# Kernel tuning notes

Measured on AMD Instinct MI355X. Metric: run time of the kernel, lower is better.

## Reference

```python
import jax, jax.numpy as jnp
import numpy as np

B, D, E, H, DEPTH, NH, K = 4, 384, 8, 1536, 12, 6, 2
P, NTOK = 16, 197  # patch size, 14*14 patches + cls
EPS = 1e-6


def layernorm(x, w, b):
    m = x.mean(-1, keepdims=True)
    v = ((x - m) ** 2).mean(-1, keepdims=True)
    return (x - m) / jnp.sqrt(v + EPS) * w + b


def attention(x, qkv_w, qkv_b, proj_w, proj_b):
    Bn, N, C = x.shape
    hd = C // NH
    qkv = x @ qkv_w.T + qkv_b                       # [B,N,3C]
    qkv = qkv.reshape(Bn, N, 3, NH, hd).transpose(2, 0, 3, 1, 4)
    q, k, v = qkv[0], qkv[1], qkv[2]                # [B,h,N,hd]
    attn = jax.nn.softmax((q @ k.transpose(0, 1, 3, 2)) * (hd ** -0.5), axis=-1)
    out = (attn @ v).transpose(0, 2, 1, 3).reshape(Bn, N, C)
    return out @ proj_w.T + proj_b


def mlp(x, w1, b1, w2, b2):
    h = jax.nn.gelu(x @ w1.T + b1, approximate=False)
    return h @ w2.T + b2


def moe_ffn(x2d, gw, w1, b1, w2, b2):
    # noiseless top-k gating (eval mode of NoisyTopKGating)
    logits = x2d @ gw                                # [T,E]
    T = logits.shape[0]
    top_vals, top_idx = jax.lax.top_k(logits, K + 1)
    gates_k = jax.nn.softmax(top_vals[:, :K], axis=-1)
    gates = jnp.zeros((T, E), x2d.dtype).at[jnp.arange(T)[:, None], top_idx[:, :K]].set(gates_k)
    # dense per-expert FFN, weighted combine (identical math to SparseDispatcher)
    h = jax.nn.gelu(jnp.einsum('td,edh->teh', x2d, w1) + b1, approximate=False)
    out = jnp.einsum('teh,ehd->ted', h, w2) + b2
    return jnp.einsum('te,ted->td', gates, out)


def forward(x, patch_w, patch_b, cls_token, pos_embed,
            ln1_w, ln1_b, qkv_w, qkv_b, proj_w, proj_b, ln2_w, ln2_b,
            fc1_w, fc1_b, fc2_w, fc2_b,
            gate_w, moe_w1, moe_b1, moe_w2, moe_b2, lnf_w, lnf_b):
    # patch embed: conv k=16 s=16
    feat = jax.lax.conv_general_dilated(x, patch_w, (P, P), 'VALID',
                                        dimension_numbers=('NCHW', 'OIHW', 'NCHW'))
    feat = feat + patch_b[None, :, None, None]
    Bn = feat.shape[0]
    tokens = feat.reshape(Bn, D, -1).transpose(0, 2, 1)          # [B,196,D]
    cls = jnp.broadcast_to(cls_token, (Bn, 1, D))
    h = jnp.concatenate([cls, tokens], axis=1) + pos_embed       # [B,197,D]

    for i in range(DEPTH):
        h = h + attention(layernorm(h, ln1_w[i], ln1_b[i]), qkv_w[i], qkv_b[i], proj_w[i], proj_b[i])
        y = layernorm(h, ln2_w[i], ln2_b[i])
        if i % 2 == 1:
            j = i // 2
            y2 = moe_ffn(y.reshape(-1, D), gate_w[j], moe_w1[j], moe_b1[j], moe_w2[j], moe_b2[j])
            h = h + y2.reshape(Bn, NTOK, D)
        else:
            j = i // 2
            h = h + mlp(y, fc1_w[j], fc1_b[j], fc2_w[j], fc2_b[j])
    return layernorm(h, lnf_w, lnf_b)


def setup_inputs() -> dict:
    key = jax.random.key(0)
    ks = jax.random.split(key, 16)
    rn = lambda k, s, sd=0.02: jax.random.normal(k, s, jnp.float32) * sd
    return {
        'x': jax.random.normal(ks[0], (B, 3, 224, 224), jnp.float32),
        'patch_w': rn(ks[1], (D, 3, P, P)), 'patch_b': jnp.zeros((D,), jnp.float32),
        'cls_token': rn(ks[2], (1, 1, D)), 'pos_embed': rn(ks[3], (1, NTOK, D)),
        'ln1_w': jnp.ones((DEPTH, D), jnp.float32), 'ln1_b': jnp.zeros((DEPTH, D), jnp.float32),
        'qkv_w': rn(ks[4], (DEPTH, 3 * D, D)), 'qkv_b': jnp.zeros((DEPTH, 3 * D), jnp.float32),
        'proj_w': rn(ks[5], (DEPTH, D, D)), 'proj_b': jnp.zeros((DEPTH, D), jnp.float32),
        'ln2_w': jnp.ones((DEPTH, D), jnp.float32), 'ln2_b': jnp.zeros((DEPTH, D), jnp.float32),
        'fc1_w': rn(ks[6], (DEPTH // 2, H, D)), 'fc1_b': jnp.zeros((DEPTH // 2, H), jnp.float32),
        'fc2_w': rn(ks[7], (DEPTH // 2, D, H)), 'fc2_b': jnp.zeros((DEPTH // 2, D), jnp.float32),
        'gate_w': rn(ks[8], (DEPTH // 2, D, E)),
        'moe_w1': rn(ks[9], (DEPTH // 2, E, D, H)), 'moe_b1': jnp.zeros((DEPTH // 2, E, H), jnp.float32),
        'moe_w2': rn(ks[10], (DEPTH // 2, E, H, D)), 'moe_b2': jnp.zeros((DEPTH // 2, E, D), jnp.float32),
        'lnf_w': jnp.ones((D,), jnp.float32), 'lnf_b': jnp.zeros((D,), jnp.float32),
    }


def reference(x, patch_w, patch_b, cls_token, pos_embed,
              ln1_w, ln1_b, qkv_w, qkv_b, proj_w, proj_b, ln2_w, ln2_b,
              fc1_w, fc1_b, fc2_w, fc2_b,
              gate_w, moe_w1, moe_b1, moe_w2, moe_b2, lnf_w, lnf_b):
    return forward(x, patch_w, patch_b, cls_token, pos_embed,
                   ln1_w, ln1_b, qkv_w, qkv_b, proj_w, proj_b, ln2_w, ln2_b,
                   fc1_w, fc1_b, fc2_w, fc2_b,
                   gate_w, moe_w1, moe_b1, moe_w2, moe_b2, lnf_w, lnf_b)
```

## Files before the change

kernel.cpp:

```cpp
#include <hip/hip_runtime.h>
#include <math.h>

#define NBATCH 4
#define NTOK 197
#define TT 788
#define DM 384
#define HM 1536
#define NHEAD 6
#define NEXP 8
#define LD2 72
#define MOUTSZ (TT * 2 * DM)

typedef __attribute__((ext_vector_type(8))) short bf16x8;
typedef __attribute__((ext_vector_type(4))) float f32x4;

__device__ __forceinline__ void f2bf2(float x, short& hi, short& lo) {
    unsigned u = __float_as_uint(x);
    unsigned uh = u + (0x7fffu + ((u >> 16) & 1u));
    hi = (short)(uh >> 16);
    float hf = __uint_as_float(uh & 0xffff0000u);
    float r = x - hf;
    unsigned v = __float_as_uint(r);
    lo = (short)((v + (0x7fffu + ((v >> 16) & 1u))) >> 16);
}
__device__ __forceinline__ float gelu_f(float x) {
    return 0.5f * x * (1.0f + erff(x * 0.7071067811865475f));
}

__global__ void k_im2col(const float* __restrict__ X, float* __restrict__ P) {
    int p = blockIdx.x;
    int b = p / 196, pp = p % 196;
    int py = pp / 14, px = pp % 14;
    const float* xb = X + (size_t)b * 3 * 224 * 224;
    float* dst = P + (size_t)p * 768;
    for (int idx = threadIdx.x; idx < 768; idx += 256) {
        int c = idx >> 8;
        int i = (idx >> 4) & 15;
        int j = idx & 15;
        dst[idx] = xb[((size_t)c * 224 + py * 16 + i) * 224 + px * 16 + j];
    }
}

__global__ void k_assemble(const float* __restrict__ PO, const float* __restrict__ pb,
                           const float* __restrict__ cls, const float* __restrict__ pos,
                           float* __restrict__ H) {
    int t = blockIdx.x;
    int b = t / NTOK, n = t % NTOK;
    for (int d = threadIdx.x; d < DM; d += 128) {
        float v;
        if (n == 0) v = cls[d];
        else v = PO[((size_t)b * 196 + (n - 1)) * DM + d] + pb[d];
        H[(size_t)t * DM + d] = v + pos[(size_t)n * DM + d];
    }
}

__global__ void k_ln(const float* __restrict__ X, const float* __restrict__ w,
                     const float* __restrict__ b, float* __restrict__ Y) {
    int t = blockIdx.x, lane = threadIdx.x;
    const float* x = X + (size_t)t * DM;
    float v[6];
    float s = 0.f;
    #pragma unroll
    for (int i = 0; i < 6; ++i) { v[i] = x[lane + i * 64]; s += v[i]; }
    #pragma unroll
    for (int off = 32; off; off >>= 1) s += __shfl_xor(s, off);
    float mean = s * (1.f / 384.f);
    float q = 0.f;
    #pragma unroll
    for (int i = 0; i < 6; ++i) { float d = v[i] - mean; q += d * d; }
    #pragma unroll
    for (int off = 32; off; off >>= 1) q += __shfl_xor(q, off);
    float inv = rsqrtf(q * (1.f / 384.f) + 1e-6f);
    float* y = Y + (size_t)t * DM;
    #pragma unroll
    for (int i = 0; i < 6; ++i) {
        int d = lane + i * 64;
        y[d] = (v[i] - mean) * inv * w[d] + b[d];
    }
}

__global__ __launch_bounds__(256) void k_gemm_mfma(
    const float* __restrict__ A, const float* __restrict__ W,
    const float* __restrict__ bias, float* __restrict__ C,
    int M, int N, int K, int flags, int MT, int NT, int wprot, int ksplit,
    const float* __restrict__ lnw, const float* __restrict__ lnb)
{
    int mt, nt, ks = 0;
    {
        int lane8 = blockIdx.x & 7;
        int idx = blockIdx.x >> 3;
        if (ksplit > 1) { ks = idx % ksplit; idx /= ksplit; }
        if (wprot) {
            mt = idx % MT;
            nt = lane8 + 8 * (idx / MT);
            if (nt >= NT) return;
        } else {
            nt = idx % NT;
            mt = lane8 + 8 * (idx / NT);
            if (mt >= MT) return;
        }
    }
    const int Ks = K / ksplit;
    const float* Ab = A + (size_t)ks * Ks;
    const float* Wb = W + (size_t)ks * Ks;
    __shared__ short Ah[64 * LD2], Al[64 * LD2], Bh[64 * LD2], Bl[64 * LD2];
    const int bm = mt * 64, bn = nt * 64;
    const int tid = threadIdx.x;
    const int lane = tid & 63, w = tid >> 6;
    const int wr = w >> 1, wc = w & 1;
    const int r16 = lane & 15, g = lane >> 4;
    const int sr = tid >> 4;
    const int sc = (tid & 15) * 4;
    const bool doln = (flags & 8) != 0;
    float am[4], ai[4];
    #pragma unroll
    for (int p = 0; p < 4; ++p) { am[p] = 0.f; ai[p] = 1.f; }
    if (doln) {
        int j = tid & 15;
        #pragma unroll
        for (int p = 0; p < 4; ++p) {
            int r = bm + sr + p * 16;
            if (r < M) {
                const float* xr = A + (size_t)r * K;
                float s = 0.f, ss = 0.f;
                #pragma unroll
                for (int i = 0; i < 6; ++i) {
                    float4 v = *(const float4*)(xr + j * 4 + i * 64);
                    s += v.x + v.y + v.z + v.w;
                    ss += v.x * v.x + v.y * v.y + v.z * v.z + v.w * v.w;
                }
                #pragma unroll
                for (int off = 1; off < 16; off <<= 1) {
                    s += __shfl_xor(s, off);
                    ss += __shfl_xor(ss, off);
                }
                float mean = s * (1.f / 384.f);
                float var = ss * (1.f / 384.f) - mean * mean;
                am[p] = mean;
                ai[p] = rsqrtf(var + 1e-6f);
            }
        }
    }
    float4 ra[4], rb[4], lw4, lb4;
    auto LOADT = [&](int k0) {
        if (doln) {
            lw4 = *(const float4*)(lnw + k0 + sc);
            lb4 = *(const float4*)(lnb + k0 + sc);
        }
        #pragma unroll
        for (int p = 0; p < 4; ++p) {
            int r = sr + p * 16;
            ra[p] = make_float4(0.f, 0.f, 0.f, 0.f);
            if (bm + r < M) ra[p] = *(const float4*)(Ab + (size_t)(bm + r) * K + k0 + sc);
            rb[p] = *(const float4*)(Wb + (size_t)(bn + r) * K + k0 + sc);
        }
    };
    auto STORET = [&]() {
        #pragma unroll
        for (int p = 0; p < 4; ++p) {
            int r = sr + p * 16;
            float4 a4 = ra[p];
            if (doln) {
                a4.x = (a4.x - am[p]) * ai[p] * lw4.x + lb4.x;
                a4.y = (a4.y - am[p]) * ai[p] * lw4.y + lb4.y;
                a4.z = (a4.z - am[p]) * ai[p] * lw4.z + lb4.z;
                a4.w = (a4.w - am[p]) * ai[p] * lw4.w + lb4.w;
            }
            float4 b4 = rb[p];
            short4 ah, al, bh, bl;
            f2bf2(a4.x, ah.x, al.x); f2bf2(a4.y, ah.y, al.y);
            f2bf2(a4.z, ah.z, al.z); f2bf2(a4.w, ah.w, al.w);
            f2bf2(b4.x, bh.x, bl.x); f2bf2(b4.y, bh.y, bl.y);
            f2bf2(b4.z, bh.z, bl.z); f2bf2(b4.w, bh.w, bl.w);
            *(short4*)&Ah[r * LD2 + sc] = ah; *(short4*)&Al[r * LD2 + sc] = al;
            *(short4*)&Bh[r * LD2 + sc] = bh; *(short4*)&Bl[r * LD2 + sc] = bl;
        }
    };
    f32x4 acc[2][2] = {};
    auto COMPUTE = [&]() {
        #pragma unroll
        for (int kk = 0; kk < 2; ++kk) {
            bf16x8 afh[2], afl[2], bfh[2], bfl[2];
            #pragma unroll
            for (int i = 0; i < 2; ++i) {
                int off = (wr * 32 + i * 16 + r16) * LD2 + kk * 32 + g * 8;
                afh[i] = *(const bf16x8*)&Ah[off];
                afl[i] = *(const bf16x8*)&Al[off];
            }
            #pragma unroll
            for (int j = 0; j < 2; ++j) {
                int off = (wc * 32 + j * 16 + r16) * LD2 + kk * 32 + g * 8;
                bfh[j] = *(const bf16x8*)&Bh[off];
                bfl[j] = *(const bf16x8*)&Bl[off];
            }
            #pragma unroll
            for (int i = 0; i < 2; ++i)
                #pragma unroll
                for (int j = 0; j < 2; ++j) {
                    acc[i][j] = __builtin_amdgcn_mfma_f32_16x16x32_bf16(afl[i], bfh[j], acc[i][j], 0, 0, 0);
                    acc[i][j] = __builtin_amdgcn_mfma_f32_16x16x32_bf16(afh[i], bfl[j], acc[i][j], 0, 0, 0);
                    acc[i][j] = __builtin_amdgcn_mfma_f32_16x16x32_bf16(afh[i], bfh[j], acc[i][j], 0, 0, 0);
                }
        }
    };
    LOADT(0);
    STORET();
    __syncthreads();
    for (int k0 = 64; k0 < Ks; k0 += 64) {
        LOADT(k0);
        COMPUTE();
        __syncthreads();
        STORET();
        __syncthreads();
    }
    COMPUTE();
    #pragma unroll
    for (int i = 0; i < 2; ++i) {
        #pragma unroll
        for (int j = 0; j < 2; ++j) {
            int n = bn + wc * 32 + j * 16 + r16;
            float bb = (bias && ks == 0) ? bias[n] : 0.f;
            int mbase = bm + wr * 32 + i * 16 + g * 4;
            #pragma unroll
            for (int r = 0; r < 4; ++r) {
                int m = mbase + r;
                if (m < M) {
                    float v = acc[i][j][r] + bb;
                    float* cp = C + (size_t)m * N + n;
                    if (flags & 16) {
                        atomicAdd(cp, v);
                    } else {
                        if (flags & 1) v = gelu_f(v);
                        if (flags & 2) v += *cp;
                        *cp = v;
                    }
                }
            }
        }
    }
}

__global__ __launch_bounds__(256) void k_scoresm(const float* __restrict__ QKV,
                                                 float* __restrict__ S) {
    int z = blockIdx.y;
    int b = z / NHEAD, hh = z % NHEAD;
    int i0 = blockIdx.x * 32;
    __shared__ float qs[32][65];
    __shared__ float ks[32][65];
    __shared__ float srow[32][200];
    int tid = threadIdx.x;
    int r = tid >> 3, d0 = (tid & 7) * 8, c0 = (tid & 7) * 4, l8 = tid & 7;
    {
        float4 v0 = make_float4(0,0,0,0), v1 = v0;
        if (i0 + r < NTOK) {
            const float* qp = QKV + ((size_t)(b * NTOK + i0 + r)) * 1152 + hh * 64 + d0;
            v0 = *(const float4*)qp; v1 = *(const float4*)(qp + 4);
        }
        qs[r][d0+0]=v0.x; qs[r][d0+1]=v0.y; qs[r][d0+2]=v0.z; qs[r][d0+3]=v0.w;
        qs[r][d0+4]=v1.x; qs[r][d0+5]=v1.y; qs[r][d0+6]=v1.z; qs[r][d0+7]=v1.w;
    }
    if (l8 == 0) { srow[r][197] = -1e30f; srow[r][198] = -1e30f; srow[r][199] = -1e30f; }
    for (int j0 = 0; j0 < NTOK; j0 += 32) {
        __syncthreads();
        {
            float4 v0 = make_float4(0,0,0,0), v1 = v0;
            if (j0 + r < NTOK) {
                const float* kp = QKV + ((size_t)(b * NTOK + j0 + r)) * 1152 + 384 + hh * 64 + d0;
                v0 = *(const float4*)kp; v1 = *(const float4*)(kp + 4);
            }
            ks[r][d0+0]=v0.x; ks[r][d0+1]=v0.y; ks[r][d0+2]=v0.z; ks[r][d0+3]=v0.w;
            ks[r][d0+4]=v1.x; ks[r][d0+5]=v1.y; ks[r][d0+6]=v1.z; ks[r][d0+7]=v1.w;
        }
        __syncthreads();
        float acc[4] = {0.f, 0.f, 0.f, 0.f};
        #pragma unroll 8
        for (int d = 0; d < 64; ++d) {
            float qv = qs[r][d];
            #pragma unroll
            for (int u = 0; u < 4; ++u) acc[u] += qv * ks[c0 + u][d];
        }
        #pragma unroll
        for (int u = 0; u < 4; ++u) {
            int j = j0 + c0 + u;
            if (j < NTOK) srow[r][j] = acc[u] * 0.125f;
        }
    }
    __syncthreads();
    float m = -1e30f;
    for (int c = l8; c < 200; c += 8) m = fmaxf(m, srow[r][c]);
    #pragma unroll
    for (int off = 1; off < 8; off <<= 1) m = fmaxf(m, __shfl_xor(m, off));
    float s = 0.f;
    for (int c = l8; c < 200; c += 8) {
        float e = expf(srow[r][c] - m);
        srow[r][c] = e;
        s += e;
    }
    #pragma unroll
    for (int off = 1; off < 8; off <<= 1) s += __shfl_xor(s, off);
    float invs = 1.f / s;
    int i = i0 + r;
    if (i < NTOK) {
        float* sp = S + ((size_t)z * NTOK + i) * NTOK;
        for (int c = l8; c < NTOK; c += 8) sp[c] = srow[r][c] * invs;
    }
}

__global__ __launch_bounds__(256) void k_pv(const float* __restrict__ S, const float* __restrict__ QKV,
                                            float* __restrict__ AO) {
    int z = blockIdx.y;
    int b = z / NHEAD, hh = z % NHEAD;
    int i0 = blockIdx.x * 32;
    __shared__ float ps[32][33];
    __shared__ float vs[32][65];
    int tid = threadIdx.x;
    int r = tid >> 3;
    int c4 = (tid & 7) * 4;
    int d0 = (tid & 7) * 8;
    float acc[8] = {};
    for (int k0 = 0; k0 < NTOK; k0 += 32) {
        #pragma unroll
        for (int u = 0; u < 4; ++u) {
            int i = i0 + r, j = k0 + c4 + u;
            ps[r][c4 + u] = (i < NTOK && j < NTOK) ? S[((size_t)z * NTOK + i) * NTOK + j] : 0.f;
        }
        {
            float4 v0 = make_float4(0,0,0,0), v1 = v0;
            if (k0 + r < NTOK) {
                const float* vp = QKV + ((size_t)(b * NTOK + k0 + r)) * 1152 + 768 + hh * 64 + d0;
                v0 = *(const float4*)vp; v1 = *(const float4*)(vp + 4);
            }
            vs[r][d0+0]=v0.x; vs[r][d0+1]=v0.y; vs[r][d0+2]=v0.z; vs[r][d0+3]=v0.w;
            vs[r][d0+4]=v1.x; vs[r][d0+5]=v1.y; vs[r][d0+6]=v1.z; vs[r][d0+7]=v1.w;
        }
        __syncthreads();
        #pragma unroll 8
        for (int kk = 0; kk < 32; ++kk) {
            float pw = ps[r][kk];
            #pragma unroll
            for (int j = 0; j < 8; ++j) acc[j] += pw * vs[kk][d0 + j];
        }
        __syncthreads();
    }
    int i = i0 + r;
    if (i < NTOK) {
        float* op = AO + (size_t)(b * NTOK + i) * DM + hh * 64 + d0;
        #pragma unroll
        for (int j = 0; j < 8; ++j) op[j] = acc[j];
    }
}

__global__ void k_route_ln(const float* __restrict__ H, float* __restrict__ lnstat,
                           const float* __restrict__ lnw, const float* __restrict__ lnb,
                           const float* __restrict__ GW,
                           int* __restrict__ eidx, float* __restrict__ egate) {
    int t = blockIdx.x * 4 + (threadIdx.x >> 6);
    if (t >= TT) return;
    int lane = threadIdx.x & 63;
    const float* x = H + (size_t)t * DM;
    float v[6];
    float s = 0.f, ss = 0.f;
    #pragma unroll
    for (int i = 0; i < 6; ++i) {
        v[i] = x[lane + i * 64];
        s += v[i];
        ss += v[i] * v[i];
    }
    #pragma unroll
    for (int off = 32; off; off >>= 1) { s += __shfl_xor(s, off); ss += __shfl_xor(ss, off); }
    float mean = s * (1.f / 384.f);
    float var = ss * (1.f / 384.f) - mean * mean;
    float inv = rsqrtf(var + 1e-6f);
    if (lane == 0) { lnstat[2 * t] = mean; lnstat[2 * t + 1] = inv; }
    float l8v[NEXP] = {};
    #pragma unroll
    for (int i = 0; i < 6; ++i) {
        int d = lane + i * 64;
        float yv = (v[i] - mean) * inv * lnw[d] + lnb[d];
        const float* g = GW + (size_t)d * NEXP;
        #pragma unroll
        for (int e = 0; e < NEXP; ++e) l8v[e] += yv * g[e];
    }
    #pragma unroll
    for (int e = 0; e < NEXP; ++e) {
        float vv = l8v[e];
        #pragma unroll
        for (int off = 32; off; off >>= 1) vv += __shfl_xor(vv, off);
        l8v[e] = vv;
    }
    if (lane == 0) {
        int b0 = 0;
        #pragma unroll
        for (int e = 1; e < NEXP; ++e) if (l8v[e] > l8v[b0]) b0 = e;
        int b1 = -1;
        #pragma unroll
        for (int e = 0; e < NEXP; ++e) if (e != b0 && (b1 < 0 || l8v[e] > l8v[b1])) b1 = e;
        float e1 = expf(l8v[b1] - l8v[b0]);
        float denom = 1.f + e1;
        eidx[2 * t] = b0; eidx[2 * t + 1] = b1;
        egate[2 * t] = 1.f / denom; egate[2 * t + 1] = e1 / denom;
    }
}

__global__ void k_pscatter(int* __restrict__ cnt, int* __restrict__ basep,
                           const int* __restrict__ eidx,
                           int* __restrict__ slot_tok, int* __restrict__ slot_of) {
    __shared__ int hist[NEXP];
    __shared__ int bp[NEXP];
    __shared__ int fl[NEXP];
    int tid = threadIdx.x;
    if (tid < NEXP) { hist[tid] = 0; fl[tid] = 0; }
    __syncthreads();
    for (int i = tid; i < 2 * TT; i += 256) atomicAdd(&hist[eidx[i]], 1);
    __syncthreads();
    if (tid == 0) {
        int s = 0;
        for (int e = 0; e < NEXP; ++e) { bp[e] = s; s += hist[e]; }
    }
    __syncthreads();
    if (tid < NEXP) { cnt[tid] = hist[tid]; basep[tid] = bp[tid]; }
    for (int t = tid; t < TT; t += 256) {
        #pragma unroll
        for (int k = 0; k < 2; ++k) {
            int e = eidx[2 * t + k];
            int pos = atomicAdd(&fl[e], 1);
            int s = bp[e] + pos;
            slot_tok[s] = t;
            slot_of[2 * t + k] = s;
        }
    }
}

__global__ __launch_bounds__(256) void k_moe1_mfma(
    const float* __restrict__ H, const float* __restrict__ lnstat,
    const float* __restrict__ lnw, const float* __restrict__ lnb,
    const float* __restrict__ W1, const float* __restrict__ B1,
    const int* __restrict__ slot_tok, const int* __restrict__ cnt, const int* __restrict__ basep,
    float* __restrict__ HID)
{
    const int e = blockIdx.x & 7;
    const int idx = blockIdx.x >> 3;
    const int mt = idx % 13;
    const int nt = idx / 13;
    const int c = cnt[e];
    const int r0 = mt * 64;
    if (r0 >= c) return;
    const int sbase = basep[e];
    const int n0 = nt * 64;
    const float* W = W1 + (size_t)e * DM * HM;
    const float* B1e = B1 + (size_t)e * HM;
    __shared__ short Ah[64 * LD2], Al[64 * LD2], Bh[64 * LD2], Bl[64 * LD2];
    const int tid = threadIdx.x;
    const int lane = tid & 63, w = tid >> 6;
    const int wr = w >> 1, wc = w & 1;
    const int r16 = lane & 15, g = lane >> 4;
    const int sr = tid >> 4, sc = (tid & 15) * 4;
    const int kq = (tid >> 4) * 4;
    int tokp[4];
    float am4[4], ai4[4];
    #pragma unroll
    for (int p = 0; p < 4; ++p) {
        int m = r0 + sr + p * 16;
        tokp[p] = (m < c) ? slot_tok[sbase + m] : -1;
        am4[p] = 0.f; ai4[p] = 1.f;
        if (tokp[p] >= 0) { am4[p] = lnstat[2 * tokp[p]]; ai4[p] = lnstat[2 * tokp[p] + 1]; }
    }
    f32x4 acc[2][2] = {};
    for (int k0 = 0; k0 < DM; k0 += 64) {
        float4 lw4 = *(const float4*)(lnw + k0 + sc);
        float4 lb4 = *(const float4*)(lnb + k0 + sc);
        #pragma unroll
        for (int p = 0; p < 4; ++p) {
            int r = sr + p * 16;
            float4 a4 = make_float4(0.f, 0.f, 0.f, 0.f);
            if (tokp[p] >= 0) {
                a4 = *(const float4*)(H + (size_t)tokp[p] * DM + k0 + sc);
                a4.x = (a4.x - am4[p]) * ai4[p] * lw4.x + lb4.x;
                a4.y = (a4.y - am4[p]) * ai4[p] * lw4.y + lb4.y;
                a4.z = (a4.z - am4[p]) * ai4[p] * lw4.z + lb4.z;
                a4.w = (a4.w - am4[p]) * ai4[p] * lw4.w + lb4.w;
            }
            short4 ah, al;
            f2bf2(a4.x, ah.x, al.x); f2bf2(a4.y, ah.y, al.y);
            f2bf2(a4.z, ah.z, al.z); f2bf2(a4.w, ah.w, al.w);
            *(short4*)&Ah[r * LD2 + sc] = ah; *(short4*)&Al[r * LD2 + sc] = al;
        }
        {
            float4 b4[4];
            #pragma unroll
            for (int i = 0; i < 4; ++i)
                b4[i] = *(const float4*)(W + (size_t)(k0 + kq + i) * HM + n0 + sc);
            float col[4][4] = {
                { b4[0].x, b4[1].x, b4[2].x, b4[3].x },
                { b4[0].y, b4[1].y, b4[2].y, b4[3].y },
                { b4[0].z, b4[1].z, b4[2].z, b4[3].z },
                { b4[0].w, b4[1].w, b4[2].w, b4[3].w } };
            #pragma unroll
            for (int u = 0; u < 4; ++u) {
                short4 hh, ll;
                f2bf2(col[u][0], hh.x, ll.x); f2bf2(col[u][1], hh.y, ll.y);
                f2bf2(col[u][2], hh.z, ll.z); f2bf2(col[u][3], hh.w, ll.w);
                *(short4*)&Bh[(sc + u) * LD2 + kq] = hh;
                *(short4*)&Bl[(sc + u) * LD2 + kq] = ll;
            }
        }
        __syncthreads();
        #pragma unroll
        for (int kk = 0; kk < 2; ++kk) {
            bf16x8 afh[2], afl[2], bfh[2], bfl[2];
            #pragma unroll
            for (int i = 0; i < 2; ++i) {
                int off = (wr * 32 + i * 16 + r16) * LD2 + kk * 32 + g * 8;
                afh[i] = *(const bf16x8*)&Ah[off];
                afl[i] = *(const bf16x8*)&Al[off];
            }
            #pragma unroll
            for (int j = 0; j < 2; ++j) {
                int off = (wc * 32 + j * 16 + r16) * LD2 + kk * 32 + g * 8;
                bfh[j] = *(const bf16x8*)&Bh[off];
                bfl[j] = *(const bf16x8*)&Bl[off];
            }
            #pragma unroll
            for (int i = 0; i < 2; ++i)
                #pragma unroll
                for (int j = 0; j < 2; ++j) {
                    acc[i][j] = __builtin_amdgcn_mfma_f32_16x16x32_bf16(afl[i], bfh[j], acc[i][j], 0, 0, 0);
                    acc[i][j] = __builtin_amdgcn_mfma_f32_16x16x32_bf16(afh[i], bfl[j], acc[i][j], 0, 0, 0);
                    acc[i][j] = __builtin_amdgcn_mfma_f32_16x16x32_bf16(afh[i], bfh[j], acc[i][j], 0, 0, 0);
                }
        }
        __syncthreads();
    }
    #pragma unroll
    for (int i = 0; i < 2; ++i) {
        #pragma unroll
        for (int j = 0; j < 2; ++j) {
            int n = n0 + wc * 32 + j * 16 + r16;
            float bb = B1e[n];
            #pragma unroll
            for (int r = 0; r < 4; ++r) {
                int m = r0 + wr * 32 + i * 16 + g * 4 + r;
                if (m < c)
                    HID[(size_t)(sbase + m) * HM + n] = gelu_f(acc[i][j][r] + bb);
            }
        }
    }
}

__global__ __launch_bounds__(256) void k_moe2_mfma(
    const float* __restrict__ HID, const float* __restrict__ W2,
    const int* __restrict__ cnt, const int* __restrict__ basep,
    float* __restrict__ MOUTP)
{
    const int e = blockIdx.x & 7;
    const int idx = blockIdx.x >> 3;
    const int mt = idx % 13;
    const int rest = idx / 13;
    const int nt = rest % 6;
    const int ks = rest / 6;
    const int c = cnt[e];
    const int r0 = mt * 64;
    if (r0 >= c) return;
    const int sbase = basep[e];
    const int n0 = nt * 64;
    const int kbase = ks * 384;
    const float* W = W2 + (size_t)e * HM * DM + (size_t)kbase * DM;
    float* outp = MOUTP + (size_t)ks * MOUTSZ;
    __shared__ short Ah[64 * LD2], Al[64 * LD2], Bh[64 * LD2], Bl[64 * LD2];
    const int tid = threadIdx.x;
    const int lane = tid & 63, w = tid >> 6;
    const int wr = w >> 1, wc = w & 1;
    const int r16 = lane & 15, g = lane >> 4;
    const int sr = tid >> 4, sc = (tid & 15) * 4;
    const int kq = (tid >> 4) * 4;
    f32x4 acc[2][2] = {};
    for (int k0 = 0; k0 < 384; k0 += 64) {
        #pragma unroll
        for (int p = 0; p < 4; ++p) {
            int r = sr + p * 16;
            int m = r0 + r;
            float4 a4 = make_float4(0.f, 0.f, 0.f, 0.f);
            if (m < c) a4 = *(const float4*)(HID + (size_t)(sbase + m) * HM + kbase + k0 + sc);
            short4 ah, al;
            f2bf2(a4.x, ah.x, al.x); f2bf2(a4.y, ah.y, al.y);
            f2bf2(a4.z, ah.z, al.z); f2bf2(a4.w, ah.w, al.w);
            *(short4*)&Ah[r * LD2 + sc] = ah; *(short4*)&Al[r * LD2 + sc] = al;
        }
        {
            float4 b4[4];
            #pragma unroll
            for (int i = 0; i < 4; ++i)
                b4[i] = *(const float4*)(W + (size_t)(k0 + kq + i) * DM + n0 + sc);
            float col[4][4] = {
                { b4[0].x, b4[1].x, b4[2].x, b4[3].x },
                { b4[0].y, b4[1].y, b4[2].y, b4[3].y },
                { b4[0].z, b4[1].z, b4[2].z, b4[3].z },
                { b4[0].w, b4[1].w, b4[2].w, b4[3].w } };
            #pragma unroll
            for (int u = 0; u < 4; ++u) {
                short4 hh, ll;
                f2bf2(col[u][0], hh.x, ll.x); f2bf2(col[u][1], hh.y, ll.y);
                f2bf2(col[u][2], hh.z, ll.z); f2bf2(col[u][3], hh.w, ll.w);
                *(short4*)&Bh[(sc + u) * LD2 + kq] = hh;
                *(short4*)&Bl[(sc + u) * LD2 + kq] = ll;
            }
        }
        __syncthreads();
        #pragma unroll
        for (int kk = 0; kk < 2; ++kk) {
            bf16x8 afh[2], afl[2], bfh[2], bfl[2];
            #pragma unroll
            for (int i = 0; i < 2; ++i) {
                int off = (wr * 32 + i * 16 + r16) * LD2 + kk * 32 + g * 8;
                afh[i] = *(const bf16x8*)&Ah[off];
                afl[i] = *(const bf16x8*)&Al[off];
            }
            #pragma unroll
            for (int j = 0; j < 2; ++j) {
                int off = (wc * 32 + j * 16 + r16) * LD2 + kk * 32 + g * 8;
                bfh[j] = *(const bf16x8*)&Bh[off];
                bfl[j] = *(const bf16x8*)&Bl[off];
            }
            #pragma unroll
            for (int i = 0; i < 2; ++i)
                #pragma unroll
                for (int j = 0; j < 2; ++j) {
                    acc[i][j] = __builtin_amdgcn_mfma_f32_16x16x32_bf16(afl[i], bfh[j], acc[i][j], 0, 0, 0);
                    acc[i][j] = __builtin_amdgcn_mfma_f32_16x16x32_bf16(afh[i], bfl[j], acc[i][j], 0, 0, 0);
                    acc[i][j] = __builtin_amdgcn_mfma_f32_16x16x32_bf16(afh[i], bfh[j], acc[i][j], 0, 0, 0);
                }
        }
        __syncthreads();
    }
    #pragma unroll
    for (int i = 0; i < 2; ++i) {
        #pragma unroll
        for (int j = 0; j < 2; ++j) {
            int n = n0 + wc * 32 + j * 16 + r16;
            #pragma unroll
            for (int r = 0; r < 4; ++r) {
                int m = r0 + wr * 32 + i * 16 + g * 4 + r;
                if (m < c)
                    outp[(size_t)(sbase + m) * DM + n] = acc[i][j][r];
            }
        }
    }
}

__global__ void k_combine(const float* __restrict__ MOUTP, const int* __restrict__ slot_of,
                          const int* __restrict__ eidx, const float* __restrict__ egate,
                          const float* __restrict__ B2, float* __restrict__ H) {
    int t = blockIdx.x;
    int s0 = slot_of[2 * t], s1 = slot_of[2 * t + 1];
    int e0 = eidx[2 * t], e1 = eidx[2 * t + 1];
    float g0 = egate[2 * t], g1 = egate[2 * t + 1];
    for (int d = threadIdx.x; d < DM; d += 128) {
        float v0 = B2[(size_t)e0 * DM + d];
        float v1 = B2[(size_t)e1 * DM + d];
        #pragma unroll
        for (int p = 0; p < 4; ++p) {
            v0 += MOUTP[(size_t)p * MOUTSZ + (size_t)s0 * DM + d];
            v1 += MOUTP[(size_t)p * MOUTSZ + (size_t)s1 * DM + d];
        }
        H[(size_t)t * DM + d] += g0 * v0 + g1 * v1;
    }
}

extern "C" void kernel_launch(void* const* d_in, const int* in_sizes, int n_in,
                              void* d_out, int out_size, void* d_ws, size_t ws_size,
                              hipStream_t stream) {
    const float* x         = (const float*)d_in[0];
    const float* patch_w   = (const float*)d_in[1];
    const float* patch_b   = (const float*)d_in[2];
    const float* cls_token = (const float*)d_in[3];
    const float* pos_embed = (const float*)d_in[4];
    const float* ln1_w     = (const float*)d_in[5];
    const float* ln1_b     = (const float*)d_in[6];
    const float* qkv_w     = (const float*)d_in[7];
    const float* qkv_b     = (const float*)d_in[8];
    const float* proj_w    = (const float*)d_in[9];
    const float* proj_b    = (const float*)d_in[10];
    const float* ln2_w     = (const float*)d_in[11];
    const float* ln2_b     = (const float*)d_in[12];
    const float* fc1_w     = (const float*)d_in[13];
    const float* fc1_b     = (const float*)d_in[14];
    const float* fc2_w     = (const float*)d_in[15];
    const float* fc2_b     = (const float*)d_in[16];
    const float* gate_w    = (const float*)d_in[17];
    const float* moe_w1    = (const float*)d_in[18];
    const float* moe_b1    = (const float*)d_in[19];
    const float* moe_w2    = (const float*)d_in[20];
    const float* moe_b2    = (const float*)d_in[21];
    const float* lnf_w     = (const float*)d_in[22];
    const float* lnf_b     = (const float*)d_in[23];
    float* out = (float*)d_out;

    float* wsf = (float*)d_ws;
    float* regA     = wsf;
    float* patches  = regA;
    float* patchout = regA + 602112;
    float* moehid   = regA;
    float* h     = regA + 2420736;
    float* spare = h + 302592;
    float* qkvb  = spare + 302592;
    float* attno = qkvb + 907776;
    float* regC  = attno + 302592;
    float* S    = regC;
    float* hid  = regC;
    float* mout4 = qkvb;
    float* egate = regC + 1210368;
    int* ib       = (int*)(egate + 1576);
    int* eidx     = ib;
    int* slot_tok = ib + 1576;
    int* slot_of  = ib + 3152;
    int* cnt      = ib + 4728;
    int* basep    = ib + 4736;
    float* lnstat = (float*)(ib + 4752);

    k_im2col<<<784, 256, 0, stream>>>(x, patches);
    k_gemm_mfma<<<96, 256, 0, stream>>>(patches, patch_w, nullptr, patchout,
                                        784, DM, 768, 0, 13, 6, 0, 1, nullptr, nullptr);
    k_assemble<<<TT, 128, 0, stream>>>(patchout, patch_b, cls_token, pos_embed, h);

    for (int l = 0; l < 12; ++l) {
        k_gemm_mfma<<<312, 256, 0, stream>>>(h, qkv_w + (size_t)l * 1152 * DM,
                                             qkv_b + l * 1152, qkvb, TT, 1152, DM, 8,
                                             13, 18, 1, 1,
                                             ln1_w + l * DM, ln1_b + l * DM);
        k_scoresm<<<dim3(7, NBATCH * NHEAD), 256, 0, stream>>>(qkvb, S);
        k_pv<<<dim3(7, NBATCH * NHEAD), 256, 0, stream>>>(S, qkvb, attno);
        k_gemm_mfma<<<192, 256, 0, stream>>>(attno, proj_w + (size_t)l * DM * DM,
                                             proj_b + l * DM, h, TT, DM, DM, 16,
                                             13, 6, 0, 2, nullptr, nullptr);
        int j = l >> 1;
        if ((l & 1) == 0) {
            k_gemm_mfma<<<312, 256, 0, stream>>>(h, fc1_w + (size_t)j * HM * DM,
                                                 fc1_b + j * HM, hid, TT, HM, DM, 9,
                                                 13, 24, 1, 1,
                                                 ln2_w + l * DM, ln2_b + l * DM);
            k_gemm_mfma<<<384, 256, 0, stream>>>(hid, fc2_w + (size_t)j * DM * HM,
                                                 fc2_b + j * DM, h, TT, DM, HM, 16,
                                                 13, 6, 0, 4, nullptr, nullptr);
        } else {
            k_route_ln<<<197, 256, 0, stream>>>(h, lnstat, ln2_w + l * DM, ln2_b + l * DM,
                                                gate_w + (size_t)j * DM * NEXP, eidx, egate);
            k_pscatter<<<1, 256, 0, stream>>>(cnt, basep, eidx, slot_tok, slot_of);
            k_moe1_mfma<<<8 * 13 * 24, 256, 0, stream>>>(
                h, lnstat, ln2_w + l * DM, ln2_b + l * DM,
                moe_w1 + (size_t)j * NEXP * DM * HM, moe_b1 + (size_t)j * NEXP * HM,
                slot_tok, cnt, basep, moehid);
            k_moe2_mfma<<<8 * 13 * 24, 256, 0, stream>>>(
                moehid, moe_w2 + (size_t)j * NEXP * HM * DM, cnt, basep, mout4);
            k_combine<<<TT, 128, 0, stream>>>(mout4, slot_of, eidx, egate,
                                              moe_b2 + (size_t)j * NEXP * DM, h);
        }
    }
    k_ln<<<TT, 64, 0, stream>>>(h, lnf_w, lnf_b, out);
}
```

Measured before the change: 1.669 ms.

## Fuse im2col and assembly into patch GEMM; fold MoE combine into expert GEMM atomics

A dedicated patch-embedding GEMM now reads image patches straight from the input and writes tokens with patch bias, position embedding and the cls row. This replaces the im2col, generic GEMM and assembly kernels. The MoE second-expert GEMM now scales its outputs by per-slot gates and atomically adds them into the residual stream, which removes the split-K partial buffer and the combine kernel. The cost is fp32 atomics onto shared rows, which also makes the summation order non-deterministic.

```diff
diff --git a/kernel.cpp b/kernel.cpp
--- a/kernel.cpp
+++ b/kernel.cpp
@@ -9,7 +9,6 @@
 #define NHEAD 6
 #define NEXP 8
 #define LD2 72
-#define MOUTSZ (TT * 2 * DM)
 
 typedef __attribute__((ext_vector_type(8))) short bf16x8;
 typedef __attribute__((ext_vector_type(4))) float f32x4;
@@ -27,33 +26,6 @@
     return 0.5f * x * (1.0f + erff(x * 0.7071067811865475f));
 }
 
-__global__ void k_im2col(const float* __restrict__ X, float* __restrict__ P) {
-    int p = blockIdx.x;
-    int b = p / 196, pp = p % 196;
-    int py = pp / 14, px = pp % 14;
-    const float* xb = X + (size_t)b * 3 * 224 * 224;
-    float* dst = P + (size_t)p * 768;
-    for (int idx = threadIdx.x; idx < 768; idx += 256) {
-        int c = idx >> 8;
-        int i = (idx >> 4) & 15;
-        int j = idx & 15;
-        dst[idx] = xb[((size_t)c * 224 + py * 16 + i) * 224 + px * 16 + j];
-    }
-}
-
-__global__ void k_assemble(const float* __restrict__ PO, const float* __restrict__ pb,
-                           const float* __restrict__ cls, const float* __restrict__ pos,
-                           float* __restrict__ H) {
-    int t = blockIdx.x;
-    int b = t / NTOK, n = t % NTOK;
-    for (int d = threadIdx.x; d < DM; d += 128) {
-        float v;
-        if (n == 0) v = cls[d];
-        else v = PO[((size_t)b * 196 + (n - 1)) * DM + d] + pb[d];
-        H[(size_t)t * DM + d] = v + pos[(size_t)n * DM + d];
-    }
-}
-
 __global__ void k_ln(const float* __restrict__ X, const float* __restrict__ w,
                      const float* __restrict__ b, float* __restrict__ Y) {
     int t = blockIdx.x, lane = threadIdx.x;
@@ -76,6 +48,126 @@
     for (int i = 0; i < 6; ++i) {
         int d = lane + i * 64;
         y[d] = (v[i] - mean) * inv * w[d] + b[d];
+    }
+}
+
+__global__ __launch_bounds__(256) void k_patch_gemm(
+    const float* __restrict__ X, const float* __restrict__ W,
+    const float* __restrict__ pb, const float* __restrict__ cls,
+    const float* __restrict__ pos, float* __restrict__ H)
+{
+    const int M = 784, N = 384, K = 768, MT = 13, NT = 6;
+    int mt, nt;
+    {
+        int lane8 = blockIdx.x & 7;
+        int idx = blockIdx.x >> 3;
+        nt = idx % NT;
+        mt = lane8 + 8 * (idx / NT);
+        if (mt >= MT) return;
+    }
+    __shared__ short Ah[64 * LD2], Al[64 * LD2], Bh[64 * LD2], Bl[64 * LD2];
+    const int bm = mt * 64, bn = nt * 64;
+    const int tid = threadIdx.x;
+    const int lane = tid & 63, w = tid >> 6;
+    const int wr = w >> 1, wc = w & 1;
+    const int r16 = lane & 15, g = lane >> 4;
+    const int sr = tid >> 4;
+    const int sc = (tid & 15) * 4;
+    const float* cvb[4];
+    bool aok[4];
+    #pragma unroll
+    for (int p = 0; p < 4; ++p) {
+        int row = bm + sr + p * 16;
+        aok[p] = row < M;
+        int b = row / 196, pp = row % 196;
+        int py = pp / 14, px = pp % 14;
+        cvb[p] = X + (size_t)b * 150528 + (size_t)(py * 16) * 224 + px * 16;
+    }
+    float4 ra[4], rb[4];
+    auto LOADT = [&](int k0) {
+        int k = k0 + sc;
+        int c = k >> 8, ii = (k >> 4) & 15, j = k & 15;
+        size_t coff = (size_t)c * 50176 + ii * 224 + j;
+        #pragma unroll
+        for (int p = 0; p < 4; ++p) {
+            ra[p] = aok[p] ? *(const float4*)(cvb[p] + coff) : make_float4(0.f, 0.f, 0.f, 0.f);
+            rb[p] = *(const float4*)(W + (size_t)(bn + sr + p * 16) * K + k0 + sc);
+        }
+    };
+    auto STORET = [&]() {
+        #pragma unroll
+        for (int p = 0; p < 4; ++p) {
+            int r = sr + p * 16;
+            float4 a4 = ra[p], b4 = rb[p];
+            short4 ah, al, bh, bl;
+            f2bf2(a4.x, ah.x, al.x); f2bf2(a4.y, ah.y, al.y);
+            f2bf2(a4.z, ah.z, al.z); f2bf2(a4.w, ah.w, al.w);
+            f2bf2(b4.x, bh.x, bl.x); f2bf2(b4.y, bh.y, bl.y);
+            f2bf2(b4.z, bh.z, bl.z); f2bf2(b4.w, bh.w, bl.w);
+            *(short4*)&Ah[r * LD2 + sc] = ah; *(short4*)&Al[r * LD2 + sc] = al;
+            *(short4*)&Bh[r * LD2 + sc] = bh; *(short4*)&Bl[r * LD2 + sc] = bl;
+        }
+    };
+    f32x4 acc[2][2] = {};
+    auto COMPUTE = [&]() {
+        #pragma unroll
+        for (int kk = 0; kk < 2; ++kk) {
+            bf16x8 afh[2], afl[2], bfh[2], bfl[2];
+            #pragma unroll
+            for (int i = 0; i < 2; ++i) {
+                int off = (wr * 32 + i * 16 + r16) * LD2 + kk * 32 + g * 8;
+                afh[i] = *(const bf16x8*)&Ah[off];
+                afl[i] = *(const bf16x8*)&Al[off];
+            }
+            #pragma unroll
+            for (int j = 0; j < 2; ++j) {
+                int off = (wc * 32 + j * 16 + r16) * LD2 + kk * 32 + g * 8;
+                bfh[j] = *(const bf16x8*)&Bh[off];
+                bfl[j] = *(const bf16x8*)&Bl[off];
+            }
+            #pragma unroll
+            for (int i = 0; i < 2; ++i)
+                #pragma unroll
+                for (int j = 0; j < 2; ++j) {
+                    acc[i][j] = __builtin_amdgcn_mfma_f32_16x16x32_bf16(afl[i], bfh[j], acc[i][j], 0, 0, 0);
+                    acc[i][j] = __builtin_amdgcn_mfma_f32_16x16x32_bf16(afh[i], bfl[j], acc[i][j], 0, 0, 0);
+                    acc[i][j] = __builtin_amdgcn_mfma_f32_16x16x32_bf16(afh[i], bfh[j], acc[i][j], 0, 0, 0);
+                }
+        }
+    };
+    LOADT(0);
+    STORET();
+    __syncthreads();
+    for (int k0 = 64; k0 < K; k0 += 64) {
+        LOADT(k0);
+        COMPUTE();
+        __syncthreads();
+        STORET();
+        __syncthreads();
+    }
+    COMPUTE();
+    #pragma unroll
+    for (int i = 0; i < 2; ++i) {
+        #pragma unroll
+        for (int j = 0; j < 2; ++j) {
+            int n = bn + wc * 32 + j * 16 + r16;
+            int mbase = bm + wr * 32 + i * 16 + g * 4;
+            #pragma unroll
+            for (int r = 0; r < 4; ++r) {
+                int m = mbase + r;
+                if (m < M) {
+                    int b = m / 196, pp = m % 196;
+                    int t = b * NTOK + 1 + pp;
+                    H[(size_t)t * DM + n] = acc[i][j][r] + pb[n] + pos[(size_t)(1 + pp) * DM + n];
+                }
+            }
+        }
+    }
+    if (blockIdx.x == 0) {
+        for (int idx = tid; idx < NBATCH * DM; idx += 256) {
+            int b = idx / DM, d = idx % DM;
+            H[(size_t)(b * NTOK) * DM + d] = cls[d] + pos[d];
+        }
     }
 }
 
@@ -403,8 +495,8 @@
 }
 
 __global__ void k_pscatter(int* __restrict__ cnt, int* __restrict__ basep,
-                           const int* __restrict__ eidx,
-                           int* __restrict__ slot_tok, int* __restrict__ slot_of) {
+                           const int* __restrict__ eidx, const float* __restrict__ egate,
+                           int* __restrict__ slot_tok, float* __restrict__ slot_gate) {
     __shared__ int hist[NEXP];
     __shared__ int bp[NEXP];
     __shared__ int fl[NEXP];
@@ -426,7 +518,7 @@
             int pos = atomicAdd(&fl[e], 1);
             int s = bp[e] + pos;
             slot_tok[s] = t;
-            slot_of[2 * t + k] = s;
+            slot_gate[s] = egate[2 * t + k];
         }
     }
 }
@@ -548,9 +640,10 @@
 }
 
 __global__ __launch_bounds__(256) void k_moe2_mfma(
-    const float* __restrict__ HID, const float* __restrict__ W2,
+    const float* __restrict__ HID, const float* __restrict__ W2, const float* __restrict__ B2,
     const int* __restrict__ cnt, const int* __restrict__ basep,
-    float* __restrict__ MOUTP)
+    const int* __restrict__ slot_tok, const float* __restrict__ slot_gate,
+    float* __restrict__ H)
 {
     const int e = blockIdx.x & 7;
     const int idx = blockIdx.x >> 3;
@@ -565,7 +658,7 @@
     const int n0 = nt * 64;
     const int kbase = ks * 384;
     const float* W = W2 + (size_t)e * HM * DM + (size_t)kbase * DM;
-    float* outp = MOUTP + (size_t)ks * MOUTSZ;
+    const float* B2e = B2 + (size_t)e * DM;
     __shared__ short Ah[64 * LD2], Al[64 * LD2], Bh[64 * LD2], Bl[64 * LD2];
     const int tid = threadIdx.x;
     const int lane = tid & 63, w = tid >> 6;
@@ -637,32 +730,17 @@
         #pragma unroll
         for (int j = 0; j < 2; ++j) {
             int n = n0 + wc * 32 + j * 16 + r16;
+            float bb = (ks == 0) ? B2e[n] : 0.f;
             #pragma unroll
             for (int r = 0; r < 4; ++r) {
                 int m = r0 + wr * 32 + i * 16 + g * 4 + r;
-                if (m < c)
-                    outp[(size_t)(sbase + m) * DM + n] = acc[i][j][r];
-            }
-        }
-    }
-}
-
-__global__ void k_combine(const float* __restrict__ MOUTP, const int* __restrict__ slot_of,
-                          const int* __restrict__ eidx, const float* __restrict__ egate,
-                          const float* __restrict__ B2, float* __restrict__ H) {
-    int t = blockIdx.x;
-    int s0 = slot_of[2 * t], s1 = slot_of[2 * t + 1];
-    int e0 = eidx[2 * t], e1 = eidx[2 * t + 1];
-    float g0 = egate[2 * t], g1 = egate[2 * t + 1];
-    for (int d = threadIdx.x; d < DM; d += 128) {
-        float v0 = B2[(size_t)e0 * DM + d];
-        float v1 = B2[(size_t)e1 * DM + d];
-        #pragma unroll
-        for (int p = 0; p < 4; ++p) {
-            v0 += MOUTP[(size_t)p * MOUTSZ + (size_t)s0 * DM + d];
-            v1 += MOUTP[(size_t)p * MOUTSZ + (size_t)s1 * DM + d];
-        }
-        H[(size_t)t * DM + d] += g0 * v0 + g1 * v1;
+                if (m < c) {
+                    int tok = slot_tok[sbase + m];
+                    float gt = slot_gate[sbase + m];
+                    atomicAdd(&H[(size_t)tok * DM + n], gt * (acc[i][j][r] + bb));
+                }
+            }
+        }
     }
 }
 
@@ -697,8 +775,6 @@
 
     float* wsf = (float*)d_ws;
     float* regA     = wsf;
-    float* patches  = regA;
-    float* patchout = regA + 602112;
     float* moehid   = regA;
     float* h     = regA + 2420736;
     float* spare = h + 302592;
@@ -707,7 +783,6 @@
     float* regC  = attno + 302592;
     float* S    = regC;
     float* hid  = regC;
-    float* mout4 = qkvb;
     float* egate = regC + 1210368;
     int* ib       = (int*)(egate + 1576);
     int* eidx     = ib;
@@ -716,11 +791,9 @@
     int* cnt      = ib + 4728;
     int* basep    = ib + 4736;
     float* lnstat = (float*)(ib + 4752);
-
-    k_im2col<<<784, 256, 0, stream>>>(x, patches);
-    k_gemm_mfma<<<96, 256, 0, stream>>>(patches, patch_w, nullptr, patchout,
-                                        784, DM, 768, 0, 13, 6, 0, 1, nullptr, nullptr);
-    k_assemble<<<TT, 128, 0, stream>>>(patchout, patch_b, cls_token, pos_embed, h);
+    float* slot_gate = lnstat + 1576;
+
+    k_patch_gemm<<<96, 256, 0, stream>>>(x, patch_w, patch_b, cls_token, pos_embed, h);
 
     for (int l = 0; l < 12; ++l) {
         k_gemm_mfma<<<312, 256, 0, stream>>>(h, qkv_w + (size_t)l * 1152 * DM,
@@ -744,15 +817,14 @@
         } else {
             k_route_ln<<<197, 256, 0, stream>>>(h, lnstat, ln2_w + l * DM, ln2_b + l * DM,
                                                 gate_w + (size_t)j * DM * NEXP, eidx, egate);
-            k_pscatter<<<1, 256, 0, stream>>>(cnt, basep, eidx, slot_tok, slot_of);
+            k_pscatter<<<1, 256, 0, stream>>>(cnt, basep, eidx, egate, slot_tok, slot_gate);
             k_moe1_mfma<<<8 * 13 * 24, 256, 0, stream>>>(
                 h, lnstat, ln2_w + l * DM, ln2_b + l * DM,
                 moe_w1 + (size_t)j * NEXP * DM * HM, moe_b1 + (size_t)j * NEXP * HM,
                 slot_tok, cnt, basep, moehid);
             k_moe2_mfma<<<8 * 13 * 24, 256, 0, stream>>>(
-                moehid, moe_w2 + (size_t)j * NEXP * HM * DM, cnt, basep, mout4);
-            k_combine<<<TT, 128, 0, stream>>>(mout4, slot_of, eidx, egate,
-                                              moe_b2 + (size_t)j * NEXP * DM, h);
+                moehid, moe_w2 + (size_t)j * NEXP * HM * DM, moe_b2 + (size_t)j * NEXP * DM,
+                cnt, basep, slot_tok, slot_gate, h);
         }
     }
     k_ln<<<TT, 64, 0, stream>>>(h, lnf_w, lnf_b, out);
```

After: 1.681 ms. About the same (+0.7%).
